# Kernel optimization log

Measured on AMD Instinct MI355X. Metric: run time of the kernel, lower is better.

## Reference

```python
import jax, jax.numpy as jnp
import numpy as np

B, T, C, H, L, V = 64, 256, 256, 8, 6, 96
EPS = 1e-5


def _layernorm(x, w, b):
    m = x.mean(-1, keepdims=True)
    v = x.var(-1, keepdims=True)
    return (x - m) / jnp.sqrt(v + EPS) * w + b


def setup_inputs() -> dict:
    key = jax.random.key(0)
    ks = jax.random.split(key, 16)
    s = 0.05
    n = lambda k, sh: jax.random.normal(k, sh, jnp.float32) * s
    return {
        'idx': jax.random.randint(ks[0], (B, T), 0, V),
        'target': jax.random.randint(ks[1], (B, T), 0, V),
        'tok_emb': n(ks[2], (V, C)),
        'pos_emb': n(ks[3], (T, C)),
        'Wq': n(ks[4], (L, C, C)),
        'Wk': n(ks[5], (L, C, C)),
        'Wv': n(ks[6], (L, C, C)),
        'Wo': n(ks[7], (L, C, C)),
        'bo': jnp.zeros((L, C), jnp.float32),
        'W1': n(ks[8], (L, C, C)),
        'b1': jnp.zeros((L, C), jnp.float32),
        'W2': n(ks[9], (L, C, C)),
        'b2': jnp.zeros((L, C), jnp.float32),
        'ln1_w': jnp.ones((L, C), jnp.float32),
        'ln1_b': jnp.zeros((L, C), jnp.float32),
        'ln2_w': jnp.ones((L, C), jnp.float32),
        'ln2_b': jnp.zeros((L, C), jnp.float32),
        'lnf_w': jnp.ones((C,), jnp.float32),
        'lnf_b': jnp.zeros((C,), jnp.float32),
        'Wlm': n(ks[10], (C, V)),
        'blm': jnp.zeros((V,), jnp.float32),
    }


def _forward(idx, target, tok_emb, pos_emb, Wq, Wk, Wv, Wo, bo, W1, b1, W2, b2,
             ln1_w, ln1_b, ln2_w, ln2_b, lnf_w, lnf_b, Wlm, blm):
    Bc, Tc = idx.shape
    hs = C // H
    scale = C ** (-0.5)  # NOTE: original scales by n_embed**-0.5, not head_size**-0.5
    x = tok_emb[idx] + pos_emb[:Tc]              # [B,T,C]
    causal = jnp.tril(jnp.ones((Tc, Tc), bool))  # [T,T]
    for l in range(L):
        q = (x @ Wq[l]).reshape(Bc, Tc, H, hs)
        k = (x @ Wk[l]).reshape(Bc, Tc, H, hs)
        v = (x @ Wv[l]).reshape(Bc, Tc, H, hs)
        w = jnp.einsum('bqhd,bkhd->bhqk', q, k) * scale
        w = jnp.where(causal, w, -jnp.inf)
        w = jax.nn.softmax(w, axis=-1)
        att = jnp.einsum('bhqk,bkhd->bqhd', w, v).reshape(Bc, Tc, C)
        x = _layernorm(x + att @ Wo[l] + bo[l], ln1_w[l], ln1_b[l])  # post-residual LN
        h = jax.nn.relu(x @ W1[l] + b1[l]) @ W2[l] + b2[l]
        x = _layernorm(x + h, ln2_w[l], ln2_b[l])
    x = _layernorm(x, lnf_w, lnf_b)
    logits = (x @ Wlm + blm).reshape(Bc * Tc, V)
    logp = jax.nn.log_softmax(logits, axis=-1)
    nll = -jnp.take_along_axis(logp, target.reshape(-1, 1), axis=1)
    loss = nll.mean()
    return logits, loss


def reference(idx, target, tok_emb, pos_emb, Wq, Wk, Wv, Wo, bo, W1, b1, W2, b2,
              ln1_w, ln1_b, ln2_w, ln2_b, lnf_w, lnf_b, Wlm, blm):
    return _forward(idx, target, tok_emb, pos_emb, Wq, Wk, Wv, Wo, bo, W1, b1, W2, b2,
                    ln1_w, ln1_b, ln2_w, ln2_b, lnf_w, lnf_b, Wlm, blm)
```

## Files before the change

kernel.cpp:

```cpp
#include <hip/hip_runtime.h>

typedef unsigned short u16;

#define NT   16384
#define CDIM 256
#define LAYERS 6

using bf16x8 = __attribute__((ext_vector_type(8))) __bf16;
using f32x4  = __attribute__((ext_vector_type(4))) float;

__device__ __forceinline__ u16 f2bf(float x){
  unsigned u = __float_as_uint(x);
  u += 0x7fffu + ((u >> 16) & 1u);
  return (u16)(u >> 16);
}
__device__ __forceinline__ float bf2f(u16 u){
  return __uint_as_float(((unsigned)u) << 16);
}

__device__ __forceinline__ void gll16(const u16* g, u16* l){
  __builtin_amdgcn_global_load_lds(
      (const __attribute__((address_space(1))) unsigned int*)g,
      (__attribute__((address_space(3))) unsigned int*)l, 16, 0, 0);
}

__global__ __launch_bounds__(256) void wconv_k(
    const float* __restrict__ Wq, const float* __restrict__ Wk,
    const float* __restrict__ Wv, const float* __restrict__ Wo,
    const float* __restrict__ W1, const float* __restrict__ W2,
    const float* __restrict__ Wlm, u16* __restrict__ WT)
{
  __shared__ float tile[64][65];
  const int z = blockIdx.z;
  const float* src; u16* dst; int N = 256, Npad = 256;
  if (z < 18){
    const int l = z / 3, which = z % 3;
    const float* a[3] = {Wq, Wk, Wv};
    src = a[which] + (size_t)l * 65536;
    dst = WT + (size_t)l * 196608 + (size_t)which * 65536;
  } else if (z < 36){
    const int i = z - 18, j = i / 6, l = i % 6;
    const float* a[3] = {Wo, W1, W2};
    src = a[j] + (size_t)l * 65536;
    dst = WT + 1179648 + (size_t)(j * 6 + l) * 65536;
  } else {
    src = Wlm; dst = WT + 2359296; N = 96; Npad = 128;
  }
  const int n0 = blockIdx.y * 64, k0 = blockIdx.x * 64;
  if (n0 >= Npad) return;
  const int c = threadIdx.x & 63, r0 = threadIdx.x >> 6;
  #pragma unroll
  for (int i = 0; i < 16; ++i){
    const int r = r0 + i * 4;
    tile[r][c] = (n0 + c < N) ? src[(size_t)(k0 + r) * N + n0 + c] : 0.f;
  }
  __syncthreads();
  #pragma unroll
  for (int i = 0; i < 16; ++i){
    const int cp = r0 + i * 4;
    dst[(size_t)(n0 + cp) * CDIM + k0 + c] = f2bf(tile[c][cp]);
  }
}

__global__ __launch_bounds__(256) void embed_k(
    const int* __restrict__ idx, const float* __restrict__ tok,
    const float* __restrict__ pos, u16* __restrict__ X)
{
  const int w = threadIdx.x >> 6, l = threadIdx.x & 63;
  const int r = blockIdx.x * 4 + w;
  const int id = idx[r];
  float4 tv = *reinterpret_cast<const float4*>(tok + (size_t)id * CDIM + l * 4);
  float4 pv = *reinterpret_cast<const float4*>(pos + (size_t)(r & 255) * CDIM + l * 4);
  union { u16 u[4]; uint2 q; } p;
  p.u[0] = f2bf(tv.x + pv.x); p.u[1] = f2bf(tv.y + pv.y);
  p.u[2] = f2bf(tv.z + pv.z); p.u[3] = f2bf(tv.w + pv.w);
  *reinterpret_cast<uint2*>(X + (size_t)r * CDIM + l * 4) = p.q;
}

template<int TM, int TN, int WR, int WC, bool BIAS, bool RELU, bool RES, bool LN, bool F32OUT>
__global__ __launch_bounds__(WR * WC * 64) void gemm2_k(
    const u16* __restrict__ A, const u16* __restrict__ WT,
    const float* __restrict__ bias, const u16* __restrict__ res,
    void* __restrict__ outp, const float* __restrict__ lnw,
    const float* __restrict__ lnb, int N, int ldo)
{
  constexpr int THREADS = WR * WC * 64;
  constexpr int MR = TM / (WR * 16), NR = TN / (WC * 16);
  __shared__ u16 As[TM * 256];
  const int t = threadIdx.x, l = t & 63, w = t >> 6;
  const int wr = w / WC, wc = w % WC;
  const int m0 = blockIdx.x * TM, n0 = blockIdx.y * TN;
  const int lr = l & 15, lk = (l >> 4) * 8;
  const int rb = wr * (TM / WR), cb = wc * (TN / WC);
  f32x4 acc[MR][NR] = {};

  #pragma unroll
  for (int i = 0; i < TM * 32 / THREADS; ++i){
    const int eo = (i * THREADS + t) * 8;
    gll16(A + (size_t)(m0 + (eo >> 8)) * 256 + (eo & 255), As + eo);
  }
  __syncthreads();

  #pragma unroll
  for (int kk = 0; kk < 256; kk += 32){
    bf16x8 af[MR], bf[NR];
    #pragma unroll
    for (int m = 0; m < MR; ++m)
      af[m] = *reinterpret_cast<const bf16x8*>(&As[(rb + m * 16 + lr) * 256 + kk + lk]);
    #pragma unroll
    for (int n = 0; n < NR; ++n)
      bf[n] = *reinterpret_cast<const bf16x8*>(WT + (size_t)(n0 + cb + n * 16 + lr) * 256 + kk + lk);
    #pragma unroll
    for (int m = 0; m < MR; ++m)
      #pragma unroll
      for (int n = 0; n < NR; ++n)
        acc[m][n] = __builtin_amdgcn_mfma_f32_16x16x32_bf16(af[m], bf[n], acc[m][n], 0, 0, 0);
  }

  const int rj = (l >> 4) * 4;
  if constexpr (LN){
    __shared__ float redS[TM][WC + 1], redQ[TM][WC + 1];
    #pragma unroll
    for (int m = 0; m < MR; ++m){
      #pragma unroll
      for (int j = 0; j < 4; ++j){
        const int lrow = rb + m * 16 + rj + j;
        const int grow = m0 + lrow;
        float s = 0.f, q = 0.f;
        #pragma unroll
        for (int n = 0; n < NR; ++n){
          const int gcol = cb + n * 16 + lr;
          float v = acc[m][n][j] + bias[gcol] + bf2f(res[(size_t)grow * CDIM + gcol]);
          acc[m][n][j] = v;
          s += v; q += v * v;
        }
        #pragma unroll
        for (int o = 1; o < 16; o <<= 1){ s += __shfl_xor(s, o); q += __shfl_xor(q, o); }
        if (lr == 0){ redS[lrow][wc] = s; redQ[lrow][wc] = q; }
      }
    }
    __syncthreads();
    #pragma unroll
    for (int m = 0; m < MR; ++m){
      #pragma unroll
      for (int j = 0; j < 4; ++j){
        const int lrow = rb + m * 16 + rj + j;
        const int grow = m0 + lrow;
        float s = 0.f, q = 0.f;
        #pragma unroll
        for (int c = 0; c < WC; ++c){ s += redS[lrow][c]; q += redQ[lrow][c]; }
        const float mean = s * (1.f / 256.f);
        const float rstd = rsqrtf(q * (1.f / 256.f) - mean * mean + 1e-5f);
        #pragma unroll
        for (int n = 0; n < NR; ++n){
          const int gcol = cb + n * 16 + lr;
          const float y = (acc[m][n][j] - mean) * rstd * lnw[gcol] + lnb[gcol];
          ((u16*)outp)[(size_t)grow * CDIM + gcol] = f2bf(y);
        }
      }
    }
  } else {
    #pragma unroll
    for (int m = 0; m < MR; ++m){
      #pragma unroll
      for (int n = 0; n < NR; ++n){
        const int gcol = n0 + cb + n * 16 + lr;
        if (gcol < N){
          #pragma unroll
          for (int j = 0; j < 4; ++j){
            const int grow = m0 + rb + m * 16 + rj + j;
            const size_t o = (size_t)grow * ldo + gcol;
            float v = acc[m][n][j];
            if (BIAS) v += bias[gcol];
            if (RES)  v += bf2f(res[o]);
            if (RELU) v = fmaxf(v, 0.f);
            if (F32OUT) ((float*)outp)[o] = v;
            else        ((u16*)outp)[o] = f2bf(v);
          }
        }
      }
    }
  }
}

__global__ __launch_bounds__(256) void attn_k(
    const u16* __restrict__ QKV, u16* __restrict__ O)
{
  __shared__ u16 Vt[32][264];
  __shared__ u16 Ps[64][264];
  const int bh = blockIdx.x, b = bh >> 3, h = bh & 7;
  const size_t rbase = (size_t)b * 256 * 768;
  const int qc = h * 32, kc = 256 + h * 32, vc = 512 + h * 32;
  const int t = threadIdx.x, l = t & 63, w = t >> 6;
  const int lr = l & 15, lk = (l >> 4) * 8;

  {
    const uint4* vp = reinterpret_cast<const uint4*>(QKV + rbase + (size_t)t * 768 + vc);
    #pragma unroll
    for (int i = 0; i < 4; ++i){
      union { uint4 q; u16 u[8]; } p; p.q = vp[i];
      #pragma unroll
      for (int j = 0; j < 8; ++j) Vt[i * 8 + j][t] = p.u[j];
    }
  }
  bf16x8 kf[16];
  #pragma unroll
  for (int n = 0; n < 16; ++n)
    kf[n] = *reinterpret_cast<const bf16x8*>(QKV + rbase + (size_t)(n * 16 + lr) * 768 + kc + lk);
  __syncthreads();

  for (int c = 0; c < 4; ++c){
    const int rowb = c * 64 + w * 16;
    bf16x8 qa = *reinterpret_cast<const bf16x8*>(QKV + rbase + (size_t)(rowb + lr) * 768 + qc + lk);

    f32x4 s[16];
    #pragma unroll
    for (int n = 0; n < 16; ++n){
      f32x4 z = {};
      s[n] = __builtin_amdgcn_mfma_f32_16x16x32_bf16(qa, kf[n], z, 0, 0, 0);
    }

    float inv[4];
    const int prow = w * 16 + (l >> 4) * 4;
    #pragma unroll
    for (int j = 0; j < 4; ++j){
      const int qrow = rowb + (l >> 4) * 4 + j;
      float sv[16]; float mx = -1e30f;
      #pragma unroll
      for (int n = 0; n < 16; ++n){
        float vv = s[n][j] * 0.0625f;
        sv[n] = ((n * 16 + lr) <= qrow) ? vv : -1e30f;
        mx = fmaxf(mx, sv[n]);
      }
      #pragma unroll
      for (int o = 1; o < 16; o <<= 1) mx = fmaxf(mx, __shfl_xor(mx, o));
      float sum = 0.f;
      #pragma unroll
      for (int n = 0; n < 16; ++n){
        float p = __expf(sv[n] - mx);
        sum += p;
        Ps[prow + j][n * 16 + lr] = f2bf(p);
      }
      #pragma unroll
      for (int o = 1; o < 16; o <<= 1) sum += __shfl_xor(sum, o);
      inv[j] = 1.f / sum;
    }
    __syncthreads();

    f32x4 o0 = {}, o1 = {};
    #pragma unroll
    for (int kc2 = 0; kc2 < 8; ++kc2){
      bf16x8 pa = *reinterpret_cast<const bf16x8*>(&Ps[w * 16 + lr][kc2 * 32 + lk]);
      bf16x8 v0 = *reinterpret_cast<const bf16x8*>(&Vt[lr][kc2 * 32 + lk]);
      bf16x8 v1 = *reinterpret_cast<const bf16x8*>(&Vt[16 + lr][kc2 * 32 + lk]);
      o0 = __builtin_amdgcn_mfma_f32_16x16x32_bf16(pa, v0, o0, 0, 0, 0);
      o1 = __builtin_amdgcn_mfma_f32_16x16x32_bf16(pa, v1, o1, 0, 0, 0);
    }
    #pragma unroll
    for (int j = 0; j < 4; ++j){
      const int qrow = rowb + (l >> 4) * 4 + j;
      u16* op = O + (size_t)(b * 256 + qrow) * CDIM + h * 32;
      op[lr]      = f2bf(o0[j] * inv[j]);
      op[16 + lr] = f2bf(o1[j] * inv[j]);
    }
    __syncthreads();
  }
}

__global__ __launch_bounds__(256) void lnf_k(
    const u16* __restrict__ in, const float* __restrict__ w,
    const float* __restrict__ b, u16* __restrict__ out)
{
  const int wv = threadIdx.x >> 6, l = threadIdx.x & 63;
  const int r = blockIdx.x * 4 + wv;
  union { uint2 q; u16 u[4]; } iv;
  iv.q = *reinterpret_cast<const uint2*>(in + (size_t)r * CDIM + l * 4);
  float v0 = bf2f(iv.u[0]), v1 = bf2f(iv.u[1]), v2 = bf2f(iv.u[2]), v3 = bf2f(iv.u[3]);
  float s = v0 + v1 + v2 + v3;
  float q = v0 * v0 + v1 * v1 + v2 * v2 + v3 * v3;
  #pragma unroll
  for (int o = 32; o; o >>= 1){ s += __shfl_xor(s, o); q += __shfl_xor(q, o); }
  const float mean = s * (1.f / 256.f);
  const float rstd = rsqrtf(q * (1.f / 256.f) - mean * mean + 1e-5f);
  float4 w4 = *reinterpret_cast<const float4*>(w + l * 4);
  float4 b4 = *reinterpret_cast<const float4*>(b + l * 4);
  union { u16 u[4]; uint2 q2; } p;
  p.u[0] = f2bf((v0 - mean) * rstd * w4.x + b4.x);
  p.u[1] = f2bf((v1 - mean) * rstd * w4.y + b4.y);
  p.u[2] = f2bf((v2 - mean) * rstd * w4.z + b4.z);
  p.u[3] = f2bf((v3 - mean) * rstd * w4.w + b4.w);
  *reinterpret_cast<uint2*>(out + (size_t)r * CDIM + l * 4) = p.q2;
}

__global__ __launch_bounds__(256) void nll_k(
    const float* __restrict__ logits, const int* __restrict__ target,
    float* __restrict__ nll)
{
  const int w = threadIdx.x >> 6, l = threadIdx.x & 63;
  const int r = blockIdx.x * 4 + w;
  const float* row = logits + (size_t)r * 96;
  float v0 = row[l];
  float v1 = (l < 32) ? row[64 + l] : -1e30f;
  float m = fmaxf(v0, v1);
  #pragma unroll
  for (int o = 32; o; o >>= 1) m = fmaxf(m, __shfl_xor(m, o));
  float s = __expf(v0 - m) + ((l < 32) ? __expf(v1 - m) : 0.f);
  #pragma unroll
  for (int o = 32; o; o >>= 1) s += __shfl_xor(s, o);
  if (l == 0) nll[r] = logf(s) + m - row[target[r]];
}

__global__ __launch_bounds__(256) void loss_k(
    const float* __restrict__ nll, float* __restrict__ out)
{
  __shared__ float rs[4];
  float s = 0.f;
  for (int i = threadIdx.x; i < NT; i += 256) s += nll[i];
  #pragma unroll
  for (int o = 32; o; o >>= 1) s += __shfl_xor(s, o);
  if ((threadIdx.x & 63) == 0) rs[threadIdx.x >> 6] = s;
  __syncthreads();
  if (threadIdx.x == 0) out[0] = (rs[0] + rs[1] + rs[2] + rs[3]) * (1.f / 16384.f);
}

extern "C" void kernel_launch(void* const* d_in, const int* in_sizes, int n_in,
                              void* d_out, int out_size, void* d_ws, size_t ws_size,
                              hipStream_t stream)
{
  const int*   idx    = (const int*)  d_in[0];
  const int*   target = (const int*)  d_in[1];
  const float* tok    = (const float*)d_in[2];
  const float* pos    = (const float*)d_in[3];
  const float* Wq     = (const float*)d_in[4];
  const float* Wk     = (const float*)d_in[5];
  const float* Wv     = (const float*)d_in[6];
  const float* Wo     = (const float*)d_in[7];
  const float* bo     = (const float*)d_in[8];
  const float* W1     = (const float*)d_in[9];
  const float* b1     = (const float*)d_in[10];
  const float* W2     = (const float*)d_in[11];
  const float* b2     = (const float*)d_in[12];
  const float* ln1w   = (const float*)d_in[13];
  const float* ln1b   = (const float*)d_in[14];
  const float* ln2w   = (const float*)d_in[15];
  const float* ln2b   = (const float*)d_in[16];
  const float* lnfw   = (const float*)d_in[17];
  const float* lnfb   = (const float*)d_in[18];
  const float* blm    = (const float*)d_in[20];
  float* out = (float*)d_out;

  char* ws = (char*)d_ws;
  u16*   X   = (u16*)  (ws);
  u16*   QKV = (u16*)  (ws + ( 8u << 20));
  u16*   O   = (u16*)  (ws + (32u << 20));
  u16*   hB  = (u16*)  (ws + (40u << 20));
  u16*   Xf  = (u16*)  (ws + (48u << 20));
  u16*   WT  = (u16*)  (ws + (56u << 20));
  float* nl  = (float*)(ws + (64u << 20));

  wconv_k<<<dim3(4, 4, 37), 256, 0, stream>>>(Wq, Wk, Wv, Wo, W1, W2,
                                              (const float*)d_in[19], WT);
  embed_k<<<NT / 4, 256, 0, stream>>>(idx, tok, pos, X);

  for (int l = 0; l < LAYERS; ++l){
    const u16* wqkv = WT + (size_t)l * 196608;
    const u16* wo   = WT + 1179648 + (size_t)(0 * 6 + l) * 65536;
    const u16* w1   = WT + 1179648 + (size_t)(1 * 6 + l) * 65536;
    const u16* w2   = WT + 1179648 + (size_t)(2 * 6 + l) * 65536;

    gemm2_k<128, 128, 2, 4, false, false, false, false, false>
        <<<dim3(128, 6), 512, 0, stream>>>(
        X, wqkv, nullptr, nullptr, QKV, nullptr, nullptr, 768, 768);
    attn_k<<<512, 256, 0, stream>>>(QKV, O);
    gemm2_k<64, 256, 2, 4, true, false, true, true, false>
        <<<dim3(256, 1), 512, 0, stream>>>(
        O, wo, bo + l * 256, X, X, ln1w + l * 256, ln1b + l * 256, 256, 256);
    gemm2_k<64, 128, 2, 4, true, true, false, false, false>
        <<<dim3(256, 2), 512, 0, stream>>>(
        X, w1, b1 + l * 256, nullptr, hB, nullptr, nullptr, 256, 256);
    gemm2_k<64, 256, 2, 4, true, false, true, true, false>
        <<<dim3(256, 1), 512, 0, stream>>>(
        hB, w2, b2 + l * 256, X, X, ln2w + l * 256, ln2b + l * 256, 256, 256);
  }

  lnf_k<<<NT / 4, 256, 0, stream>>>(X, lnfw, lnfb, Xf);
  gemm2_k<64, 128, 2, 4, true, false, false, false, true>
      <<<dim3(256, 1), 512, 0, stream>>>(
      Xf, WT + 2359296, blm, nullptr, out, nullptr, nullptr, 96, 96);
  nll_k<<<NT / 4, 256, 0, stream>>>(out, target, nl);
  loss_k<<<1, 256, 0, stream>>>(nl, out + (size_t)NT * 96);
}
```

Before: 684.3 us.

## Fuse whole transformer forward into one cooperative persistent megakernel

Replaces the per-layer sequence of GEMM, attention, layernorm, embedding and loss kernels with one cooperative kernel of 256 blocks. Each block keeps its 64 rows of activations resident in LDS across all layers, and only K/V (double-buffered per layer) and the attention output go through global memory, with grid syncs between phases. This removes many launches and the global round-trips of the activations. In exchange the whole forward runs on only 256 blocks with large LDS use, so occupancy is low, and each block serially loops over all 8 heads and recomputes the full-row attention.

```diff
diff --git a/kernel.cpp b/kernel.cpp
--- a/kernel.cpp
+++ b/kernel.cpp
@@ -1,13 +1,18 @@
 #include <hip/hip_runtime.h>
+#include <hip/hip_cooperative_groups.h>
+
+namespace cg = cooperative_groups;
 
 typedef unsigned short u16;
 
 #define NT   16384
-#define CDIM 256
 #define LAYERS 6
+#define LDP  264
 
 using bf16x8 = __attribute__((ext_vector_type(8))) __bf16;
 using f32x4  = __attribute__((ext_vector_type(4))) float;
+
+#define MFMA __builtin_amdgcn_mfma_f32_16x16x32_bf16
 
 __device__ __forceinline__ u16 f2bf(float x){
   unsigned u = __float_as_uint(x);
@@ -16,12 +21,6 @@
 }
 __device__ __forceinline__ float bf2f(u16 u){
   return __uint_as_float(((unsigned)u) << 16);
-}
-
-__device__ __forceinline__ void gll16(const u16* g, u16* l){
-  __builtin_amdgcn_global_load_lds(
-      (const __attribute__((address_space(1))) unsigned int*)g,
-      (__attribute__((address_space(3))) unsigned int*)l, 16, 0, 0);
 }
 
 __global__ __launch_bounds__(256) void wconv_k(
@@ -58,269 +57,362 @@
   #pragma unroll
   for (int i = 0; i < 16; ++i){
     const int cp = r0 + i * 4;
-    dst[(size_t)(n0 + cp) * CDIM + k0 + c] = f2bf(tile[c][cp]);
-  }
-}
-
-__global__ __launch_bounds__(256) void embed_k(
-    const int* __restrict__ idx, const float* __restrict__ tok,
-    const float* __restrict__ pos, u16* __restrict__ X)
+    dst[(size_t)(n0 + cp) * 256 + k0 + c] = f2bf(tile[c][cp]);
+  }
+}
+
+template<bool LNEP>
+__device__ __forceinline__ void gemm64(
+    const u16* __restrict__ Ab, const int astride,
+    const u16* __restrict__ Bw, const float* __restrict__ bias,
+    const float* __restrict__ lnw, const float* __restrict__ lnb,
+    u16* __restrict__ XT, u16* __restrict__ Hout,
+    float* __restrict__ redA, float* __restrict__ redB,
+    const int w, const int lr, const int lk, const int rj)
 {
-  const int w = threadIdx.x >> 6, l = threadIdx.x & 63;
-  const int r = blockIdx.x * 4 + w;
-  const int id = idx[r];
-  float4 tv = *reinterpret_cast<const float4*>(tok + (size_t)id * CDIM + l * 4);
-  float4 pv = *reinterpret_cast<const float4*>(pos + (size_t)(r & 255) * CDIM + l * 4);
-  union { u16 u[4]; uint2 q; } p;
-  p.u[0] = f2bf(tv.x + pv.x); p.u[1] = f2bf(tv.y + pv.y);
-  p.u[2] = f2bf(tv.z + pv.z); p.u[3] = f2bf(tv.w + pv.w);
-  *reinterpret_cast<uint2*>(X + (size_t)r * CDIM + l * 4) = p.q;
-}
-
-template<int TM, int TN, int WR, int WC, bool BIAS, bool RELU, bool RES, bool LN, bool F32OUT>
-__global__ __launch_bounds__(WR * WC * 64) void gemm2_k(
-    const u16* __restrict__ A, const u16* __restrict__ WT,
-    const float* __restrict__ bias, const u16* __restrict__ res,
-    void* __restrict__ outp, const float* __restrict__ lnw,
-    const float* __restrict__ lnb, int N, int ldo)
-{
-  constexpr int THREADS = WR * WC * 64;
-  constexpr int MR = TM / (WR * 16), NR = TN / (WC * 16);
-  __shared__ u16 As[TM * 256];
-  const int t = threadIdx.x, l = t & 63, w = t >> 6;
-  const int wr = w / WC, wc = w % WC;
-  const int m0 = blockIdx.x * TM, n0 = blockIdx.y * TN;
-  const int lr = l & 15, lk = (l >> 4) * 8;
-  const int rb = wr * (TM / WR), cb = wc * (TN / WC);
-  f32x4 acc[MR][NR] = {};
-
-  #pragma unroll
-  for (int i = 0; i < TM * 32 / THREADS; ++i){
-    const int eo = (i * THREADS + t) * 8;
-    gll16(A + (size_t)(m0 + (eo >> 8)) * 256 + (eo & 255), As + eo);
-  }
-  __syncthreads();
-
+  const int rb = (w >> 2) * 32, cb = (w & 3) * 64, wc = w & 3;
+  f32x4 acc[2][4] = {};
   #pragma unroll
   for (int kk = 0; kk < 256; kk += 32){
-    bf16x8 af[MR], bf[NR];
-    #pragma unroll
-    for (int m = 0; m < MR; ++m)
-      af[m] = *reinterpret_cast<const bf16x8*>(&As[(rb + m * 16 + lr) * 256 + kk + lk]);
-    #pragma unroll
-    for (int n = 0; n < NR; ++n)
-      bf[n] = *reinterpret_cast<const bf16x8*>(WT + (size_t)(n0 + cb + n * 16 + lr) * 256 + kk + lk);
-    #pragma unroll
-    for (int m = 0; m < MR; ++m)
-      #pragma unroll
-      for (int n = 0; n < NR; ++n)
-        acc[m][n] = __builtin_amdgcn_mfma_f32_16x16x32_bf16(af[m], bf[n], acc[m][n], 0, 0, 0);
-  }
-
-  const int rj = (l >> 4) * 4;
-  if constexpr (LN){
-    __shared__ float redS[TM][WC + 1], redQ[TM][WC + 1];
-    #pragma unroll
-    for (int m = 0; m < MR; ++m){
+    bf16x8 af[2], bf[4];
+    #pragma unroll
+    for (int m = 0; m < 2; ++m)
+      af[m] = *reinterpret_cast<const bf16x8*>(Ab + (size_t)(rb + m*16 + lr) * astride + kk + lk);
+    #pragma unroll
+    for (int n = 0; n < 4; ++n)
+      bf[n] = *reinterpret_cast<const bf16x8*>(Bw + (size_t)(cb + n*16 + lr) * 256 + kk + lk);
+    #pragma unroll
+    for (int m = 0; m < 2; ++m)
+      #pragma unroll
+      for (int n = 0; n < 4; ++n)
+        acc[m][n] = MFMA(af[m], bf[n], acc[m][n], 0, 0, 0);
+  }
+  if (LNEP){
+    #pragma unroll
+    for (int m = 0; m < 2; ++m){
       #pragma unroll
       for (int j = 0; j < 4; ++j){
-        const int lrow = rb + m * 16 + rj + j;
-        const int grow = m0 + lrow;
+        const int row = rb + m*16 + rj + j;
         float s = 0.f, q = 0.f;
         #pragma unroll
-        for (int n = 0; n < NR; ++n){
-          const int gcol = cb + n * 16 + lr;
-          float v = acc[m][n][j] + bias[gcol] + bf2f(res[(size_t)grow * CDIM + gcol]);
+        for (int n = 0; n < 4; ++n){
+          const int col = cb + n*16 + lr;
+          float v = acc[m][n][j] + bias[col] + bf2f(XT[row*LDP + col]);
           acc[m][n][j] = v;
           s += v; q += v * v;
         }
         #pragma unroll
         for (int o = 1; o < 16; o <<= 1){ s += __shfl_xor(s, o); q += __shfl_xor(q, o); }
-        if (lr == 0){ redS[lrow][wc] = s; redQ[lrow][wc] = q; }
-      }
-    }
-    __syncthreads();
-    #pragma unroll
-    for (int m = 0; m < MR; ++m){
+        if (lr == 0){ redA[row*4 + wc] = s; redB[row*4 + wc] = q; }
+      }
+    }
+    __syncthreads();
+    #pragma unroll
+    for (int m = 0; m < 2; ++m){
       #pragma unroll
       for (int j = 0; j < 4; ++j){
-        const int lrow = rb + m * 16 + rj + j;
-        const int grow = m0 + lrow;
+        const int row = rb + m*16 + rj + j;
         float s = 0.f, q = 0.f;
         #pragma unroll
-        for (int c = 0; c < WC; ++c){ s += redS[lrow][c]; q += redQ[lrow][c]; }
-        const float mean = s * (1.f / 256.f);
-        const float rstd = rsqrtf(q * (1.f / 256.f) - mean * mean + 1e-5f);
-        #pragma unroll
-        for (int n = 0; n < NR; ++n){
-          const int gcol = cb + n * 16 + lr;
-          const float y = (acc[m][n][j] - mean) * rstd * lnw[gcol] + lnb[gcol];
-          ((u16*)outp)[(size_t)grow * CDIM + gcol] = f2bf(y);
+        for (int c = 0; c < 4; ++c){ s += redA[row*4 + c]; q += redB[row*4 + c]; }
+        const float mean = s * (1.f/256.f);
+        const float rstd = rsqrtf(q * (1.f/256.f) - mean*mean + 1e-5f);
+        #pragma unroll
+        for (int n = 0; n < 4; ++n){
+          const int col = cb + n*16 + lr;
+          XT[row*LDP + col] = f2bf((acc[m][n][j] - mean) * rstd * lnw[col] + lnb[col]);
         }
       }
     }
   } else {
     #pragma unroll
-    for (int m = 0; m < MR; ++m){
-      #pragma unroll
-      for (int n = 0; n < NR; ++n){
-        const int gcol = n0 + cb + n * 16 + lr;
-        if (gcol < N){
+    for (int m = 0; m < 2; ++m)
+      #pragma unroll
+      for (int n = 0; n < 4; ++n){
+        const int col = cb + n*16 + lr;
+        #pragma unroll
+        for (int j = 0; j < 4; ++j){
+          const int row = rb + m*16 + rj + j;
+          Hout[row*LDP + col] = f2bf(fmaxf(acc[m][n][j] + bias[col], 0.f));
+        }
+      }
+  }
+}
+
+__global__ __launch_bounds__(512) void mega_k(
+    const int* __restrict__ idx, const int* __restrict__ target,
+    const float* __restrict__ tok, const float* __restrict__ pos,
+    const u16* __restrict__ WT,
+    const float* __restrict__ bo, const float* __restrict__ b1,
+    const float* __restrict__ b2,
+    const float* __restrict__ ln1w, const float* __restrict__ ln1b,
+    const float* __restrict__ ln2w, const float* __restrict__ ln2b,
+    const float* __restrict__ lnfw, const float* __restrict__ lnfb,
+    const float* __restrict__ blm,
+    u16* __restrict__ KV0, u16* __restrict__ KV1, u16* __restrict__ Obuf,
+    float* __restrict__ nl, float* __restrict__ out)
+{
+  extern __shared__ char smem[];
+  u16* XT = (u16*)smem;
+  u16* R1 = (u16*)(smem + 33792);
+  u16* PS = (u16*)(smem + 2*33792);
+  u16* VT = (u16*)(smem + 3*33792);
+  float* redA = (float*)(smem + 3*33792 + 16896);
+  float* redB = redA + 256;
+  float* redC = redB + 256;
+
+  cg::grid_group grid = cg::this_grid();
+
+  const int t = threadIdx.x, l = t & 63, w = t >> 6;
+  const int lr = l & 15, lk = (l >> 4) * 8, rj = (l >> 4) * 4;
+  const int bi = blockIdx.x;
+  const int row0 = bi * 64;
+  const int brow = (bi >> 2) * 256;
+  const int tq0  = (bi & 3) * 64;
+
+  {
+    const int r = t >> 3, c0 = (t & 7) * 32;
+    const int gr = row0 + r;
+    const int id = idx[gr];
+    #pragma unroll
+    for (int i = 0; i < 32; i += 4){
+      float4 tv = *reinterpret_cast<const float4*>(tok + (size_t)id * 256 + c0 + i);
+      float4 pv = *reinterpret_cast<const float4*>(pos + (size_t)(gr & 255) * 256 + c0 + i);
+      union{u16 u[4]; uint2 q;} p;
+      p.u[0] = f2bf(tv.x + pv.x); p.u[1] = f2bf(tv.y + pv.y);
+      p.u[2] = f2bf(tv.z + pv.z); p.u[3] = f2bf(tv.w + pv.w);
+      *reinterpret_cast<uint2*>(XT + r*LDP + c0 + i) = p.q;
+    }
+  }
+  __syncthreads();
+
+  #pragma unroll 1
+  for (int ly = 0; ly < LAYERS; ++ly){
+    u16* KV = (ly & 1) ? KV1 : KV0;
+    const u16* wqkv = WT + (size_t)ly * 196608;
+    const u16* wo = WT + 1179648 + (size_t)(0*6+ly)*65536;
+    const u16* w1 = WT + 1179648 + (size_t)(1*6+ly)*65536;
+    const u16* w2 = WT + 1179648 + (size_t)(2*6+ly)*65536;
+
+    {
+      f32x4 acc[4][6] = {};
+      #pragma unroll
+      for (int kk = 0; kk < 256; kk += 32){
+        bf16x8 af[4], bf[6];
+        #pragma unroll
+        for (int m = 0; m < 4; ++m)
+          af[m] = *reinterpret_cast<const bf16x8*>(XT + (m*16 + lr)*LDP + kk + lk);
+        #pragma unroll
+        for (int n = 0; n < 6; ++n)
+          bf[n] = *reinterpret_cast<const bf16x8*>(wqkv + (size_t)(w*96 + n*16 + lr)*256 + kk + lk);
+        #pragma unroll
+        for (int m = 0; m < 4; ++m)
+          #pragma unroll
+          for (int n = 0; n < 6; ++n)
+            acc[m][n] = MFMA(af[m], bf[n], acc[m][n], 0, 0, 0);
+      }
+      #pragma unroll
+      for (int m = 0; m < 4; ++m)
+        #pragma unroll
+        for (int n = 0; n < 6; ++n){
+          const int col = w*96 + n*16 + lr;
           #pragma unroll
           for (int j = 0; j < 4; ++j){
-            const int grow = m0 + rb + m * 16 + rj + j;
-            const size_t o = (size_t)grow * ldo + gcol;
-            float v = acc[m][n][j];
-            if (BIAS) v += bias[gcol];
-            if (RES)  v += bf2f(res[o]);
-            if (RELU) v = fmaxf(v, 0.f);
-            if (F32OUT) ((float*)outp)[o] = v;
-            else        ((u16*)outp)[o] = f2bf(v);
+            const int row = m*16 + rj + j;
+            const u16 v = f2bf(acc[m][n][j]);
+            if (col < 256) R1[row*LDP + col] = v;
+            else KV[(size_t)(row0 + row)*512 + col - 256] = v;
           }
         }
-      }
-    }
-  }
-}
-
-__global__ __launch_bounds__(256) void attn_k(
-    const u16* __restrict__ QKV, u16* __restrict__ O)
-{
-  __shared__ u16 Vt[32][264];
-  __shared__ u16 Ps[64][264];
-  const int bh = blockIdx.x, b = bh >> 3, h = bh & 7;
-  const size_t rbase = (size_t)b * 256 * 768;
-  const int qc = h * 32, kc = 256 + h * 32, vc = 512 + h * 32;
-  const int t = threadIdx.x, l = t & 63, w = t >> 6;
-  const int lr = l & 15, lk = (l >> 4) * 8;
+    }
+    grid.sync();
+
+    {
+      const int rg = w >> 1, kh = w & 1;
+      #pragma unroll 1
+      for (int h = 0; h < 8; ++h){
+        #pragma unroll
+        for (int it = 0; it < 2; ++it){
+          const int tk = t >> 1, d0 = ((t & 1) + 2*it) * 8;
+          union{uint4 q; u16 u[8];} p;
+          p.q = *reinterpret_cast<const uint4*>(KV + (size_t)(brow + tk)*512 + 256 + h*32 + d0);
+          #pragma unroll
+          for (int k2 = 0; k2 < 8; ++k2) VT[(d0 + k2)*LDP + tk] = p.u[k2];
+        }
+        bf16x8 kf[8];
+        #pragma unroll
+        for (int n = 0; n < 8; ++n)
+          kf[n] = *reinterpret_cast<const bf16x8*>(KV + (size_t)(brow + kh*128 + n*16 + lr)*512 + h*32 + lk);
+        bf16x8 qa = *reinterpret_cast<const bf16x8*>(R1 + (rg*16 + lr)*LDP + h*32 + lk);
+        f32x4 sf[8];
+        #pragma unroll
+        for (int n = 0; n < 8; ++n){ f32x4 z = {}; sf[n] = MFMA(qa, kf[n], z, 0, 0, 0); }
+        #pragma unroll
+        for (int j = 0; j < 4; ++j){
+          const int tq = tq0 + rg*16 + rj + j;
+          float m = -1e30f;
+          #pragma unroll
+          for (int n = 0; n < 8; ++n){
+            const int tk = kh*128 + n*16 + lr;
+            float v = sf[n][j] * 0.0625f;
+            v = (tk <= tq) ? v : -1e30f;
+            sf[n][j] = v;
+            m = fmaxf(m, v);
+          }
+          #pragma unroll
+          for (int o = 1; o < 16; o <<= 1) m = fmaxf(m, __shfl_xor(m, o));
+          if (lr == 0) redA[(rg*16 + rj + j)*2 + kh] = m;
+        }
+        __syncthreads();
+        #pragma unroll
+        for (int j = 0; j < 4; ++j){
+          const int r = rg*16 + rj + j;
+          const float m = fmaxf(redA[r*2], redA[r*2 + 1]);
+          float s = 0.f;
+          #pragma unroll
+          for (int n = 0; n < 8; ++n){
+            const float p = __expf(sf[n][j] - m);
+            s += p;
+            PS[r*LDP + kh*128 + n*16 + lr] = f2bf(p);
+          }
+          #pragma unroll
+          for (int o = 1; o < 16; o <<= 1) s += __shfl_xor(s, o);
+          if (lr == 0) redB[r*2 + kh] = s;
+        }
+        __syncthreads();
+        f32x4 o4 = {};
+        #pragma unroll
+        for (int kk = 0; kk < 8; ++kk){
+          bf16x8 pa = *reinterpret_cast<const bf16x8*>(PS + (rg*16 + lr)*LDP + kk*32 + lk);
+          bf16x8 vb = *reinterpret_cast<const bf16x8*>(VT + (kh*16 + lr)*LDP + kk*32 + lk);
+          o4 = MFMA(pa, vb, o4, 0, 0, 0);
+        }
+        #pragma unroll
+        for (int j = 0; j < 4; ++j){
+          const int r = rg*16 + rj + j;
+          const float inv = 1.f / (redB[r*2] + redB[r*2 + 1]);
+          Obuf[(size_t)(row0 + r)*256 + h*32 + kh*16 + lr] = f2bf(o4[j] * inv);
+        }
+        __syncthreads();
+      }
+    }
+
+    gemm64<true >(Obuf + (size_t)row0*256, 256, wo, bo + ly*256,
+                  ln1w + ly*256, ln1b + ly*256, XT, nullptr, redA, redB, w, lr, lk, rj);
+    __syncthreads();
+    gemm64<false>(XT, LDP, w1, b1 + ly*256, nullptr, nullptr,
+                  XT, R1, redA, redB, w, lr, lk, rj);
+    __syncthreads();
+    gemm64<true >(R1, LDP, w2, b2 + ly*256,
+                  ln2w + ly*256, ln2b + ly*256, XT, nullptr, redA, redB, w, lr, lk, rj);
+    __syncthreads();
+  }
 
   {
-    const uint4* vp = reinterpret_cast<const uint4*>(QKV + rbase + (size_t)t * 768 + vc);
-    #pragma unroll
-    for (int i = 0; i < 4; ++i){
-      union { uint4 q; u16 u[8]; } p; p.q = vp[i];
-      #pragma unroll
-      for (int j = 0; j < 8; ++j) Vt[i * 8 + j][t] = p.u[j];
-    }
-  }
-  bf16x8 kf[16];
-  #pragma unroll
-  for (int n = 0; n < 16; ++n)
-    kf[n] = *reinterpret_cast<const bf16x8*>(QKV + rbase + (size_t)(n * 16 + lr) * 768 + kc + lk);
+    const int r = t >> 3, c0 = (t & 7) * 32;
+    float va[32]; float s = 0.f, q = 0.f;
+    #pragma unroll
+    for (int i = 0; i < 32; ++i){
+      va[i] = bf2f(XT[r*LDP + c0 + i]); s += va[i]; q += va[i]*va[i];
+    }
+    #pragma unroll
+    for (int o = 1; o < 8; o <<= 1){ s += __shfl_xor(s, o); q += __shfl_xor(q, o); }
+    const float mean = s * (1.f/256.f);
+    const float rstd = rsqrtf(q * (1.f/256.f) - mean*mean + 1e-5f);
+    #pragma unroll
+    for (int i = 0; i < 32; i += 4){
+      union{u16 u[4]; uint2 qq;} p;
+      #pragma unroll
+      for (int k2 = 0; k2 < 4; ++k2)
+        p.u[k2] = f2bf((va[i+k2] - mean) * rstd * lnfw[c0+i+k2] + lnfb[c0+i+k2]);
+      *reinterpret_cast<uint2*>(R1 + r*LDP + c0 + i) = p.qq;
+    }
+  }
   __syncthreads();
 
-  for (int c = 0; c < 4; ++c){
-    const int rowb = c * 64 + w * 16;
-    bf16x8 qa = *reinterpret_cast<const bf16x8*>(QKV + rbase + (size_t)(rowb + lr) * 768 + qc + lk);
-
-    f32x4 s[16];
-    #pragma unroll
-    for (int n = 0; n < 16; ++n){
-      f32x4 z = {};
-      s[n] = __builtin_amdgcn_mfma_f32_16x16x32_bf16(qa, kf[n], z, 0, 0, 0);
-    }
-
-    float inv[4];
-    const int prow = w * 16 + (l >> 4) * 4;
+  {
+    const int rg2 = w >> 1, ch = w & 1;
+    const u16* wl = WT + 2359296;
+    f32x4 acc[3] = {};
+    #pragma unroll
+    for (int kk = 0; kk < 256; kk += 32){
+      bf16x8 af = *reinterpret_cast<const bf16x8*>(R1 + (rg2*16 + lr)*LDP + kk + lk);
+      #pragma unroll
+      for (int n = 0; n < 3; ++n){
+        bf16x8 bf = *reinterpret_cast<const bf16x8*>(wl + (size_t)(ch*48 + n*16 + lr)*256 + kk + lk);
+        acc[n] = MFMA(af, bf, acc[n], 0, 0, 0);
+      }
+    }
+    #pragma unroll
+    for (int n = 0; n < 3; ++n){
+      const int col = ch*48 + n*16 + lr;
+      #pragma unroll
+      for (int j = 0; j < 4; ++j){
+        acc[n][j] += blm[col];
+        out[(size_t)(row0 + rg2*16 + rj + j)*96 + col] = acc[n][j];
+      }
+    }
     #pragma unroll
     for (int j = 0; j < 4; ++j){
-      const int qrow = rowb + (l >> 4) * 4 + j;
-      float sv[16]; float mx = -1e30f;
-      #pragma unroll
-      for (int n = 0; n < 16; ++n){
-        float vv = s[n][j] * 0.0625f;
-        sv[n] = ((n * 16 + lr) <= qrow) ? vv : -1e30f;
-        mx = fmaxf(mx, sv[n]);
-      }
-      #pragma unroll
-      for (int o = 1; o < 16; o <<= 1) mx = fmaxf(mx, __shfl_xor(mx, o));
-      float sum = 0.f;
-      #pragma unroll
-      for (int n = 0; n < 16; ++n){
-        float p = __expf(sv[n] - mx);
-        sum += p;
-        Ps[prow + j][n * 16 + lr] = f2bf(p);
-      }
-      #pragma unroll
-      for (int o = 1; o < 16; o <<= 1) sum += __shfl_xor(sum, o);
-      inv[j] = 1.f / sum;
-    }
-    __syncthreads();
-
-    f32x4 o0 = {}, o1 = {};
-    #pragma unroll
-    for (int kc2 = 0; kc2 < 8; ++kc2){
-      bf16x8 pa = *reinterpret_cast<const bf16x8*>(&Ps[w * 16 + lr][kc2 * 32 + lk]);
-      bf16x8 v0 = *reinterpret_cast<const bf16x8*>(&Vt[lr][kc2 * 32 + lk]);
-      bf16x8 v1 = *reinterpret_cast<const bf16x8*>(&Vt[16 + lr][kc2 * 32 + lk]);
-      o0 = __builtin_amdgcn_mfma_f32_16x16x32_bf16(pa, v0, o0, 0, 0, 0);
-      o1 = __builtin_amdgcn_mfma_f32_16x16x32_bf16(pa, v1, o1, 0, 0, 0);
-    }
+      const int r = rg2*16 + rj + j;
+      float m = fmaxf(fmaxf(acc[0][j], acc[1][j]), acc[2][j]);
+      #pragma unroll
+      for (int o = 1; o < 16; o <<= 1) m = fmaxf(m, __shfl_xor(m, o));
+      if (lr == 0) redA[r*2 + ch] = m;
+    }
+    __syncthreads();
     #pragma unroll
     for (int j = 0; j < 4; ++j){
-      const int qrow = rowb + (l >> 4) * 4 + j;
-      u16* op = O + (size_t)(b * 256 + qrow) * CDIM + h * 32;
-      op[lr]      = f2bf(o0[j] * inv[j]);
-      op[16 + lr] = f2bf(o1[j] * inv[j]);
-    }
-    __syncthreads();
-  }
-}
-
-__global__ __launch_bounds__(256) void lnf_k(
-    const u16* __restrict__ in, const float* __restrict__ w,
-    const float* __restrict__ b, u16* __restrict__ out)
-{
-  const int wv = threadIdx.x >> 6, l = threadIdx.x & 63;
-  const int r = blockIdx.x * 4 + wv;
-  union { uint2 q; u16 u[4]; } iv;
-  iv.q = *reinterpret_cast<const uint2*>(in + (size_t)r * CDIM + l * 4);
-  float v0 = bf2f(iv.u[0]), v1 = bf2f(iv.u[1]), v2 = bf2f(iv.u[2]), v3 = bf2f(iv.u[3]);
-  float s = v0 + v1 + v2 + v3;
-  float q = v0 * v0 + v1 * v1 + v2 * v2 + v3 * v3;
-  #pragma unroll
-  for (int o = 32; o; o >>= 1){ s += __shfl_xor(s, o); q += __shfl_xor(q, o); }
-  const float mean = s * (1.f / 256.f);
-  const float rstd = rsqrtf(q * (1.f / 256.f) - mean * mean + 1e-5f);
-  float4 w4 = *reinterpret_cast<const float4*>(w + l * 4);
-  float4 b4 = *reinterpret_cast<const float4*>(b + l * 4);
-  union { u16 u[4]; uint2 q2; } p;
-  p.u[0] = f2bf((v0 - mean) * rstd * w4.x + b4.x);
-  p.u[1] = f2bf((v1 - mean) * rstd * w4.y + b4.y);
-  p.u[2] = f2bf((v2 - mean) * rstd * w4.z + b4.z);
-  p.u[3] = f2bf((v3 - mean) * rstd * w4.w + b4.w);
-  *reinterpret_cast<uint2*>(out + (size_t)r * CDIM + l * 4) = p.q2;
-}
-
-__global__ __launch_bounds__(256) void nll_k(
-    const float* __restrict__ logits, const int* __restrict__ target,
-    float* __restrict__ nll)
-{
-  const int w = threadIdx.x >> 6, l = threadIdx.x & 63;
-  const int r = blockIdx.x * 4 + w;
-  const float* row = logits + (size_t)r * 96;
-  float v0 = row[l];
-  float v1 = (l < 32) ? row[64 + l] : -1e30f;
-  float m = fmaxf(v0, v1);
-  #pragma unroll
-  for (int o = 32; o; o >>= 1) m = fmaxf(m, __shfl_xor(m, o));
-  float s = __expf(v0 - m) + ((l < 32) ? __expf(v1 - m) : 0.f);
-  #pragma unroll
-  for (int o = 32; o; o >>= 1) s += __shfl_xor(s, o);
-  if (l == 0) nll[r] = logf(s) + m - row[target[r]];
-}
-
-__global__ __launch_bounds__(256) void loss_k(
-    const float* __restrict__ nll, float* __restrict__ out)
-{
-  __shared__ float rs[4];
-  float s = 0.f;
-  for (int i = threadIdx.x; i < NT; i += 256) s += nll[i];
-  #pragma unroll
-  for (int o = 32; o; o >>= 1) s += __shfl_xor(s, o);
-  if ((threadIdx.x & 63) == 0) rs[threadIdx.x >> 6] = s;
-  __syncthreads();
-  if (threadIdx.x == 0) out[0] = (rs[0] + rs[1] + rs[2] + rs[3]) * (1.f / 16384.f);
+      const int r = rg2*16 + rj + j;
+      const float m = fmaxf(redA[r*2], redA[r*2 + 1]);
+      float s = __expf(acc[0][j] - m) + __expf(acc[1][j] - m) + __expf(acc[2][j] - m);
+      #pragma unroll
+      for (int o = 1; o < 16; o <<= 1) s += __shfl_xor(s, o);
+      if (lr == 0) redB[r*2 + ch] = s;
+      const int tgt = target[row0 + r];
+      const int tc = tgt - ch*48;
+      if (tc >= 0 && tc < 48 && lr == (tc & 15)){
+        const int tn = tc >> 4;
+        redC[r] = (tn == 0) ? acc[0][j] : (tn == 1) ? acc[1][j] : acc[2][j];
+      }
+    }
+    __syncthreads();
+    float lsum = 0.f;
+    if (ch == 0 && lr == 0){
+      #pragma unroll
+      for (int j = 0; j < 4; ++j){
+        const int r = rg2*16 + rj + j;
+        const float m = fmaxf(redA[r*2], redA[r*2 + 1]);
+        lsum += logf(redB[r*2] + redB[r*2 + 1]) + m - redC[r];
+      }
+    }
+    #pragma unroll
+    for (int o = 1; o < 64; o <<= 1) lsum += __shfl_xor(lsum, o);
+    __syncthreads();
+    if (l == 0) redA[w] = lsum;
+    __syncthreads();
+    if (t == 0){
+      float tot = 0.f;
+      #pragma unroll
+      for (int i = 0; i < 8; ++i) tot += redA[i];
+      nl[bi] = tot;
+    }
+  }
+  grid.sync();
+  if (bi == 0){
+    float s = (t < 256) ? nl[t] : 0.f;
+    #pragma unroll
+    for (int o = 1; o < 64; o <<= 1) s += __shfl_xor(s, o);
+    __syncthreads();
+    if (l == 0) redA[w] = s;
+    __syncthreads();
+    if (t == 0){
+      float tot = 0.f;
+      #pragma unroll
+      for (int i = 0; i < 8; ++i) tot += redA[i];
+      out[(size_t)NT * 96] = tot * (1.f / NT);
+    }
+  }
 }
 
 extern "C" void kernel_launch(void* const* d_in, const int* in_sizes, int n_in,
@@ -346,47 +438,27 @@
   const float* ln2b   = (const float*)d_in[16];
   const float* lnfw   = (const float*)d_in[17];
   const float* lnfb   = (const float*)d_in[18];
+  const float* Wlm    = (const float*)d_in[19];
   const float* blm    = (const float*)d_in[20];
   float* out = (float*)d_out;
 
   char* ws = (char*)d_ws;
-  u16*   X   = (u16*)  (ws);
-  u16*   QKV = (u16*)  (ws + ( 8u << 20));
-  u16*   O   = (u16*)  (ws + (32u << 20));
-  u16*   hB  = (u16*)  (ws + (40u << 20));
-  u16*   Xf  = (u16*)  (ws + (48u << 20));
-  u16*   WT  = (u16*)  (ws + (56u << 20));
-  float* nl  = (float*)(ws + (64u << 20));
-
-  wconv_k<<<dim3(4, 4, 37), 256, 0, stream>>>(Wq, Wk, Wv, Wo, W1, W2,
-                                              (const float*)d_in[19], WT);
-  embed_k<<<NT / 4, 256, 0, stream>>>(idx, tok, pos, X);
-
-  for (int l = 0; l < LAYERS; ++l){
-    const u16* wqkv = WT + (size_t)l * 196608;
-    const u16* wo   = WT + 1179648 + (size_t)(0 * 6 + l) * 65536;
-    const u16* w1   = WT + 1179648 + (size_t)(1 * 6 + l) * 65536;
-    const u16* w2   = WT + 1179648 + (size_t)(2 * 6 + l) * 65536;
-
-    gemm2_k<128, 128, 2, 4, false, false, false, false, false>
-        <<<dim3(128, 6), 512, 0, stream>>>(
-        X, wqkv, nullptr, nullptr, QKV, nullptr, nullptr, 768, 768);
-    attn_k<<<512, 256, 0, stream>>>(QKV, O);
-    gemm2_k<64, 256, 2, 4, true, false, true, true, false>
-        <<<dim3(256, 1), 512, 0, stream>>>(
-        O, wo, bo + l * 256, X, X, ln1w + l * 256, ln1b + l * 256, 256, 256);
-    gemm2_k<64, 128, 2, 4, true, true, false, false, false>
-        <<<dim3(256, 2), 512, 0, stream>>>(
-        X, w1, b1 + l * 256, nullptr, hB, nullptr, nullptr, 256, 256);
-    gemm2_k<64, 256, 2, 4, true, false, true, true, false>
-        <<<dim3(256, 1), 512, 0, stream>>>(
-        hB, w2, b2 + l * 256, X, X, ln2w + l * 256, ln2b + l * 256, 256, 256);
-  }
-
-  lnf_k<<<NT / 4, 256, 0, stream>>>(X, lnfw, lnfb, Xf);
-  gemm2_k<64, 128, 2, 4, true, false, false, false, true>
-      <<<dim3(256, 1), 512, 0, stream>>>(
-      Xf, WT + 2359296, blm, nullptr, out, nullptr, nullptr, 96, 96);
-  nll_k<<<NT / 4, 256, 0, stream>>>(out, target, nl);
-  loss_k<<<1, 256, 0, stream>>>(nl, out + (size_t)NT * 96);
-}
+  u16*   KV0  = (u16*)(ws);
+  u16*   KV1  = (u16*)(ws + (16u << 20));
+  u16*   Obuf = (u16*)(ws + (32u << 20));
+  u16*   WT   = (u16*)(ws + (40u << 20));
+  float* nl   = (float*)(ws + (46u << 20));
+
+  wconv_k<<<dim3(4, 4, 37), 256, 0, stream>>>(Wq, Wk, Wv, Wo, W1, W2, Wlm, WT);
+
+  const u16* WTc = WT;
+  void* args[] = {
+    (void*)&idx, (void*)&target, (void*)&tok, (void*)&pos, (void*)&WTc,
+    (void*)&bo, (void*)&b1, (void*)&b2,
+    (void*)&ln1w, (void*)&ln1b, (void*)&ln2w, (void*)&ln2b,
+    (void*)&lnfw, (void*)&lnfb, (void*)&blm,
+    (void*)&KV0, (void*)&KV1, (void*)&Obuf, (void*)&nl, (void*)&out
+  };
+  hipLaunchCooperativeKernel((void*)mega_k, dim3(256), dim3(512),
+                             args, 122368, stream);
+}
```

Result: slower. 1.074 ms (+56.9%).
